# Kernel tuning notes

Measured on AMD Instinct MI355X. Metric: run time of the kernel, lower is better.

## Reference

```python
import jax, jax.numpy as jnp
import numpy as np


@jax.custom_vjp
def sign_ste(x):
    return jnp.sign(x)

def _sign_fwd(x):
    return jnp.sign(x), x

def _sign_bwd(x, g):
    # straight-through estimator: pass grad where |x| <= 1
    return (g * (jnp.abs(x) <= 1.0).astype(g.dtype),)

sign_ste.defvjp(_sign_fwd, _sign_bwd)


def setup_inputs() -> dict:
    key = jax.random.key(0)
    ks = jax.random.split(key, 4)
    B = 262144
    return {
        "x": jax.random.normal(ks[0], (B, 256), dtype=jnp.float32),
        "w1": jax.random.normal(ks[1], (128, 256), dtype=jnp.float32) * 0.1,
        "b1": jnp.zeros((128,), dtype=jnp.float32),
        "w2": jax.random.normal(ks[2], (64, 128), dtype=jnp.float32) * 0.1,
        "b2": jnp.zeros((64,), dtype=jnp.float32),
        "w3": jax.random.normal(ks[3], (1, 64), dtype=jnp.float32) * 0.1,
        "b3": jnp.zeros((1,), dtype=jnp.float32),
    }


def reference(x, w1, b1, w2, b2, w3, b3):
    # x: [B, 256]; binarized XNOR-style 3-layer MLP, training path (sigmoid out)
    h = sign_ste(x)
    h = sign_ste(h @ sign_ste(w1).T + b1)   # [B, 128]
    h = sign_ste(h @ sign_ste(w2).T + b2)   # [B, 64]
    out = h @ sign_ste(w3).T + b3            # [B, 1]
    return jax.nn.sigmoid(out)
```

## Files before the change

### kernel.cpp

```cpp
#include <hip/hip_runtime.h>
#include <stdint.h>

typedef unsigned long long u64;


__global__ __launch_bounds__(256) void pack_weights(
    const float* __restrict__ w1, const float* __restrict__ w2,
    const float* __restrict__ w3, u64* __restrict__ wp)
{
    int t = blockIdx.x * blockDim.x + threadIdx.x;
    if (t < 512) {
        int r = t >> 2, j = t & 3;
        const float* src = w1 + r * 256 + j;
        u64 word = 0;
        #pragma unroll
        for (int l = 0; l < 64; ++l)
            word |= (u64)(src[l * 4] < 0.0f) << l;
        wp[t] = word;
    } else if (t < 640) {
        int idx = t - 512;
        int r = idx >> 1, j = idx & 1;
        const float* src = w2 + r * 128 + j * 64;
        u64 word = 0;
        #pragma unroll
        for (int l = 0; l < 64; ++l)
            word |= (u64)(src[l] < 0.0f) << l;
        wp[t] = word;
    } else if (t == 640) {
        u64 word = 0;
        #pragma unroll
        for (int l = 0; l < 64; ++l)
            word |= (u64)(w3[l] < 0.0f) << l;
        wp[t] = word;
    }
}

__global__ __launch_bounds__(256) void xnor_fwd(
    const float* __restrict__ x,
    const float* __restrict__ b1, const float* __restrict__ b2,
    const float* __restrict__ b3,
    const u64* __restrict__ w1p, const u64* __restrict__ w2p,
    const u64* __restrict__ w3p,
    float* __restrict__ out, int B)
{
    const int lane = threadIdx.x & 63;
    const int wib  = threadIdx.x >> 6;
    const int wpb  = blockDim.x >> 6;
    const long long gw = (long long)blockIdx.x * wpb + wib;
    const long long nw = (long long)gridDim.x * wpb;

    u64 w1a[4], w1b[4], w2r[2];
    #pragma unroll
    for (int j = 0; j < 4; ++j) {
        w1a[j] = w1p[lane * 4 + j];
        w1b[j] = w1p[(lane + 64) * 4 + j];
    }
    w2r[0] = w2p[lane * 2 + 0];
    w2r[1] = w2p[lane * 2 + 1];
    const u64 w3w = w3p[0];
    const float b1a = b1[lane], b1b = b1[lane + 64];
    const float b2v = b2[lane];
    const float b3v = b3[0];

    for (long long row = gw; row < B; row += nw) {
        const float4 xv = *reinterpret_cast<const float4*>(x + row * 256 + (lane << 2));

        const u64 sx0 = __ballot(xv.x < 0.0f);
        const u64 sx1 = __ballot(xv.y < 0.0f);
        const u64 sx2 = __ballot(xv.z < 0.0f);
        const u64 sx3 = __ballot(xv.w < 0.0f);

        const float prod = xv.x * xv.y * xv.z * xv.w;
        const u64 zb = __ballot(prod == 0.0f);

        int pa, pb, nzx;
        if (zb == 0ull) {
            nzx = 256;
            pa = __popcll(sx0 ^ w1a[0]) + __popcll(sx1 ^ w1a[1])
               + __popcll(sx2 ^ w1a[2]) + __popcll(sx3 ^ w1a[3]);
            pb = __popcll(sx0 ^ w1b[0]) + __popcll(sx1 ^ w1b[1])
               + __popcll(sx2 ^ w1b[2]) + __popcll(sx3 ^ w1b[3]);
        } else {
            const u64 mx0 = __ballot(xv.x != 0.0f);
            const u64 mx1 = __ballot(xv.y != 0.0f);
            const u64 mx2 = __ballot(xv.z != 0.0f);
            const u64 mx3 = __ballot(xv.w != 0.0f);
            nzx = __popcll(mx0) + __popcll(mx1) + __popcll(mx2) + __popcll(mx3);
            pa = __popcll((sx0 ^ w1a[0]) & mx0) + __popcll((sx1 ^ w1a[1]) & mx1)
               + __popcll((sx2 ^ w1a[2]) & mx2) + __popcll((sx3 ^ w1a[3]) & mx3);
            pb = __popcll((sx0 ^ w1b[0]) & mx0) + __popcll((sx1 ^ w1b[1]) & mx1)
               + __popcll((sx2 ^ w1b[2]) & mx2) + __popcll((sx3 ^ w1b[3]) & mx3);
        }

        const float ta = (float)(nzx - 2 * pa) + b1a;
        const float tb = (float)(nzx - 2 * pb) + b1b;

        const u64 s1_0 = __ballot(ta < 0.0f);
        const u64 s1_1 = __ballot(tb < 0.0f);
        const u64 m1_0 = __ballot(ta != 0.0f);
        const u64 m1_1 = __ballot(tb != 0.0f);
        const int nz1 = __popcll(m1_0) + __popcll(m1_1);

        const int p2 = __popcll((s1_0 ^ w2r[0]) & m1_0)
                     + __popcll((s1_1 ^ w2r[1]) & m1_1);
        const float t2 = (float)(nz1 - 2 * p2) + b2v;

        const u64 s2 = __ballot(t2 < 0.0f);
        const u64 m2 = __ballot(t2 != 0.0f);
        const int nz2 = __popcll(m2);

        const int p3 = __popcll((s2 ^ w3w) & m2);
        const float t3 = (float)(nz2 - 2 * p3) + b3v;
        const float res = 1.0f / (1.0f + __expf(-t3));
        if (lane == 0) out[row] = res;
    }
}

extern "C" void kernel_launch(void* const* d_in, const int* in_sizes, int n_in,
                              void* d_out, int out_size, void* d_ws, size_t ws_size,
                              hipStream_t stream)
{
    const float* x  = (const float*)d_in[0];
    const float* w1 = (const float*)d_in[1];
    const float* b1 = (const float*)d_in[2];
    const float* w2 = (const float*)d_in[3];
    const float* b2 = (const float*)d_in[4];
    const float* w3 = (const float*)d_in[5];
    const float* b3 = (const float*)d_in[6];
    float* out = (float*)d_out;
    const int B = in_sizes[0] / 256;

    u64* wp = (u64*)d_ws;

    pack_weights<<<3, 256, 0, stream>>>(w1, w2, w3, wp);

    const int blocks = 2048;
    xnor_fwd<<<blocks, 256, 0, stream>>>(x, b1, b2, b3,
                                         wp, wp + 512, wp + 640, out, B);
}
```

Baseline: 55.45 us.

## Fuse weight sign-packing into main kernel via per-block ballot into LDS

Removes the separate pack_weights launch and has every block pack the binarized w1/w2/w3 sign bits into shared memory with wave ballots before processing rows. This eliminates a kernel launch and the dependency gap between the two kernels. In exchange, each of the 2048 blocks redundantly reads about 160 KB of weights (mostly L2 hits) and runs 32 serial ballot iterations per wave before starting on x.

```diff
diff --git a/kernel.cpp b/kernel.cpp
--- a/kernel.cpp
+++ b/kernel.cpp
@@ -4,63 +4,59 @@
 typedef unsigned long long u64;
 
 
-__global__ __launch_bounds__(256) void pack_weights(
-    const float* __restrict__ w1, const float* __restrict__ w2,
-    const float* __restrict__ w3, u64* __restrict__ wp)
-{
-    int t = blockIdx.x * blockDim.x + threadIdx.x;
-    if (t < 512) {
-        int r = t >> 2, j = t & 3;
-        const float* src = w1 + r * 256 + j;
-        u64 word = 0;
-        #pragma unroll
-        for (int l = 0; l < 64; ++l)
-            word |= (u64)(src[l * 4] < 0.0f) << l;
-        wp[t] = word;
-    } else if (t < 640) {
-        int idx = t - 512;
-        int r = idx >> 1, j = idx & 1;
-        const float* src = w2 + r * 128 + j * 64;
-        u64 word = 0;
-        #pragma unroll
-        for (int l = 0; l < 64; ++l)
-            word |= (u64)(src[l] < 0.0f) << l;
-        wp[t] = word;
-    } else if (t == 640) {
-        u64 word = 0;
-        #pragma unroll
-        for (int l = 0; l < 64; ++l)
-            word |= (u64)(w3[l] < 0.0f) << l;
-        wp[t] = word;
-    }
-}
-
-__global__ __launch_bounds__(256) void xnor_fwd(
+__global__ __launch_bounds__(256) void xnor_fused(
     const float* __restrict__ x,
-    const float* __restrict__ b1, const float* __restrict__ b2,
-    const float* __restrict__ b3,
-    const u64* __restrict__ w1p, const u64* __restrict__ w2p,
-    const u64* __restrict__ w3p,
+    const float* __restrict__ w1, const float* __restrict__ b1,
+    const float* __restrict__ w2, const float* __restrict__ b2,
+    const float* __restrict__ w3, const float* __restrict__ b3,
     float* __restrict__ out, int B)
 {
+    __shared__ u64 wp[641];
+
     const int lane = threadIdx.x & 63;
     const int wib  = threadIdx.x >> 6;
     const int wpb  = blockDim.x >> 6;
-    const long long gw = (long long)blockIdx.x * wpb + wib;
-    const long long nw = (long long)gridDim.x * wpb;
+
+    for (int r = wib * 32; r < wib * 32 + 32; ++r) {
+        const float4 v = *reinterpret_cast<const float4*>(w1 + r * 256 + (lane << 2));
+        const u64 s0 = __ballot(v.x < 0.0f);
+        const u64 s1 = __ballot(v.y < 0.0f);
+        const u64 s2 = __ballot(v.z < 0.0f);
+        const u64 s3 = __ballot(v.w < 0.0f);
+        if (lane == 0) {
+            wp[r * 4 + 0] = s0; wp[r * 4 + 1] = s1;
+            wp[r * 4 + 2] = s2; wp[r * 4 + 3] = s3;
+        }
+    }
+    if (wib < 2) {
+        for (int r = wib * 32; r < wib * 32 + 32; ++r) {
+            const float a = w2[r * 128 + lane];
+            const float b = w2[r * 128 + 64 + lane];
+            const u64 s0 = __ballot(a < 0.0f);
+            const u64 s1 = __ballot(b < 0.0f);
+            if (lane == 0) { wp[512 + r * 2] = s0; wp[512 + r * 2 + 1] = s1; }
+        }
+    } else if (wib == 2) {
+        const u64 s = __ballot(w3[lane] < 0.0f);
+        if (lane == 0) wp[640] = s;
+    }
+    __syncthreads();
 
     u64 w1a[4], w1b[4], w2r[2];
     #pragma unroll
     for (int j = 0; j < 4; ++j) {
-        w1a[j] = w1p[lane * 4 + j];
-        w1b[j] = w1p[(lane + 64) * 4 + j];
+        w1a[j] = wp[lane * 4 + j];
+        w1b[j] = wp[(lane + 64) * 4 + j];
     }
-    w2r[0] = w2p[lane * 2 + 0];
-    w2r[1] = w2p[lane * 2 + 1];
-    const u64 w3w = w3p[0];
+    w2r[0] = wp[512 + lane * 2 + 0];
+    w2r[1] = wp[512 + lane * 2 + 1];
+    const u64 w3w = wp[640];
     const float b1a = b1[lane], b1b = b1[lane + 64];
     const float b2v = b2[lane];
     const float b3v = b3[0];
+
+    const long long gw = (long long)blockIdx.x * wpb + wib;
+    const long long nw = (long long)gridDim.x * wpb;
 
     for (long long row = gw; row < B; row += nw) {
         const float4 xv = *reinterpret_cast<const float4*>(x + row * 256 + (lane << 2));
@@ -130,11 +126,6 @@
     float* out = (float*)d_out;
     const int B = in_sizes[0] / 256;
 
-    u64* wp = (u64*)d_ws;
-
-    pack_weights<<<3, 256, 0, stream>>>(w1, w2, w3, wp);
-
     const int blocks = 2048;
-    xnor_fwd<<<blocks, 256, 0, stream>>>(x, b1, b2, b3,
-                                         wp, wp + 512, wp + 640, out, B);
+    xnor_fused<<<blocks, 256, 0, stream>>>(x, w1, b1, w2, b2, w3, b3, out, B);
 }
```

New measurement: 71.61 us. 29.1% more time.
